# Optimization experiments

Hardware: AMD Instinct MI355X
Metric: run time of the kernel (lower is better)

## Reference

```python
import jax, jax.numpy as jnp
import numpy as np


def setup_inputs() -> dict:
    key = jax.random.key(0)
    ks = jax.random.split(key, 6)
    B, S, I, H = 64, 512, 1024, 1024
    sc = lambda *sh: 1.0 / np.sqrt(sh[0])
    return {
        "x": jax.random.normal(ks[0], (B, S, I), dtype=jnp.float32),
        "Wih": jax.random.normal(ks[1], (I, 4 * H), dtype=jnp.float32) * sc(I),
        "Whh": jax.random.normal(ks[2], (H, 4 * H), dtype=jnp.float32) * sc(H),
        "bih": jnp.zeros((4 * H,), dtype=jnp.float32),
        "bhh": jnp.zeros((4 * H,), dtype=jnp.float32),
        "Q": jax.random.normal(ks[3], (H, I), dtype=jnp.float32) * sc(H),
        "R": jax.random.normal(ks[4], (I, H), dtype=jnp.float32) * sc(I),
        "h0": jnp.zeros((B, H), dtype=jnp.float32),
        "c0": jnp.zeros((B, H), dtype=jnp.float32),
        "mog_iterations": 5,
    }


def reference(x, Wih, Whh, bih, bhh, Q, R, h0, c0, mog_iterations):
    # x: [B, S, I]; recurrence over S via lax.scan
    def step(carry, xt):
        ht, Ct = carry
        # mogrify: alternate rescaling of xt (odd i) and ht (even i)
        for i in range(1, mog_iterations + 1):
            if i % 2 == 0:
                ht = 2.0 * jax.nn.sigmoid(xt @ R) * ht
            else:
                xt = 2.0 * jax.nn.sigmoid(ht @ Q) * xt
        gates = xt @ Wih + bih + ht @ Whh + bhh  # [B, 4H]
        ig, fg, cg, og = jnp.split(gates, 4, axis=1)
        Ct = jax.nn.sigmoid(fg) * Ct + jax.nn.sigmoid(ig) * jnp.tanh(cg)
        ht = jax.nn.sigmoid(og) * jnp.tanh(Ct)
        return (ht, Ct), None

    xs = jnp.swapaxes(x, 0, 1)  # [S, B, I]
    (ht, Ct), _ = jax.lax.scan(step, (h0, c0), xs)
    return ht
```

## Files before the change

kernel.cpp:

```cpp
#include <hip/hip_runtime.h>
#include <stdint.h>

#define NBLK 256
#define NTHR 512
#define BATCH 64
#define HD 1024
#define SEQ 512

#define FLAG_STRIDE 32

typedef unsigned short u16;
typedef uint32_t u32;
typedef __attribute__((ext_vector_type(8))) short v8s;
typedef __attribute__((ext_vector_type(4))) float v4f;
typedef __attribute__((ext_vector_type(4))) unsigned int v4u;

__device__ __forceinline__ float bf2f(u16 u){
  union { float f; u32 i; } c; c.i = ((u32)u) << 16; return c.f;
}
__device__ __forceinline__ u16 f2bf(float f){
  union { float f; u32 i; } c; c.f = f;
  u32 i = c.i;
  return (u16)((i + 0x7fffu + ((i >> 16) & 1u)) >> 16);
}
__device__ __forceinline__ float sigm(float v){ return 1.f / (1.f + __expf(-v)); }

__device__ __forceinline__ u32 packf(float v){
  const u16 hi = f2bf(v);
  const u16 lo = f2bf(v - bf2f(hi));
  return (u32)hi | ((u32)lo << 16);
}
__device__ __forceinline__ float unpackf(u32 w){
  return bf2f((u16)(w & 0xffffu)) + bf2f((u16)(w >> 16));
}

__device__ __forceinline__ u32 ald(const u32* p){
  return __hip_atomic_load(p, __ATOMIC_RELAXED, __HIP_MEMORY_SCOPE_AGENT);
}
__device__ __forceinline__ void ast(u32* p, u32 v){
  __hip_atomic_store(p, v, __ATOMIC_RELAXED, __HIP_MEMORY_SCOPE_AGENT);
}
__device__ __forceinline__ int aldi(const int* p){
  return __hip_atomic_load(p, __ATOMIC_RELAXED, __HIP_MEMORY_SCOPE_AGENT);
}

__device__ __forceinline__ void ald_batch8(const u32* p, v4u r[8]){
  asm volatile(
    "global_load_dwordx4 %0, %8, off sc0 sc1\n\t"
    "global_load_dwordx4 %1, %8, off offset:16 sc0 sc1\n\t"
    "global_load_dwordx4 %2, %8, off offset:128 sc0 sc1\n\t"
    "global_load_dwordx4 %3, %8, off offset:144 sc0 sc1\n\t"
    "global_load_dwordx4 %4, %8, off offset:256 sc0 sc1\n\t"
    "global_load_dwordx4 %5, %8, off offset:272 sc0 sc1\n\t"
    "global_load_dwordx4 %6, %8, off offset:384 sc0 sc1\n\t"
    "global_load_dwordx4 %7, %8, off offset:400 sc0 sc1\n\t"
    "s_waitcnt vmcnt(0)"
    : "=&v"(r[0]), "=&v"(r[1]), "=&v"(r[2]), "=&v"(r[3]),
      "=&v"(r[4]), "=&v"(r[5]), "=&v"(r[6]), "=&v"(r[7])
    : "v"(p) : "memory");
}
__device__ __forceinline__ void ald_batch16(const u32* p, v4u r[16]){
  asm volatile(
    "global_load_dwordx4 %0, %16, off sc0 sc1\n\t"
    "global_load_dwordx4 %1, %16, off offset:16 sc0 sc1\n\t"
    "global_load_dwordx4 %2, %16, off offset:128 sc0 sc1\n\t"
    "global_load_dwordx4 %3, %16, off offset:144 sc0 sc1\n\t"
    "global_load_dwordx4 %4, %16, off offset:256 sc0 sc1\n\t"
    "global_load_dwordx4 %5, %16, off offset:272 sc0 sc1\n\t"
    "global_load_dwordx4 %6, %16, off offset:384 sc0 sc1\n\t"
    "global_load_dwordx4 %7, %16, off offset:400 sc0 sc1\n\t"
    "global_load_dwordx4 %8, %16, off offset:512 sc0 sc1\n\t"
    "global_load_dwordx4 %9, %16, off offset:528 sc0 sc1\n\t"
    "global_load_dwordx4 %10, %16, off offset:640 sc0 sc1\n\t"
    "global_load_dwordx4 %11, %16, off offset:656 sc0 sc1\n\t"
    "global_load_dwordx4 %12, %16, off offset:768 sc0 sc1\n\t"
    "global_load_dwordx4 %13, %16, off offset:784 sc0 sc1\n\t"
    "global_load_dwordx4 %14, %16, off offset:896 sc0 sc1\n\t"
    "global_load_dwordx4 %15, %16, off offset:912 sc0 sc1\n\t"
    "s_waitcnt vmcnt(0)"
    : "=&v"(r[0]), "=&v"(r[1]), "=&v"(r[2]), "=&v"(r[3]),
      "=&v"(r[4]), "=&v"(r[5]), "=&v"(r[6]), "=&v"(r[7]),
      "=&v"(r[8]), "=&v"(r[9]), "=&v"(r[10]), "=&v"(r[11]),
      "=&v"(r[12]), "=&v"(r[13]), "=&v"(r[14]), "=&v"(r[15])
    : "v"(p) : "memory");
}

struct FragPair { v8s hi; v8s lo; };
__device__ __forceinline__ FragPair splitpair(v4u w0, v4u w1){
  union { v8s v; u32 u[4]; } H, L;
#pragma unroll
  for (int i = 0; i < 2; i++){
    H.u[i]     = (w0[2*i] & 0xffffu) | (w0[2*i+1] << 16);
    L.u[i]     = (w0[2*i] >> 16)     | (w0[2*i+1] & 0xffff0000u);
    H.u[2 + i] = (w1[2*i] & 0xffffu) | (w1[2*i+1] << 16);
    L.u[2 + i] = (w1[2*i] >> 16)     | (w1[2*i+1] & 0xffff0000u);
  }
  FragPair f; f.hi = H.v; f.lo = L.v; return f;
}

__device__ __forceinline__ void gbar_all(int* flags, int target, int bid, int tid){
  __syncthreads();
  if (tid == 0)
    __hip_atomic_store(&flags[bid * FLAG_STRIDE], target, __ATOMIC_RELAXED, __HIP_MEMORY_SCOPE_AGENT);
  if (tid < 64){
    const int* p = flags + (tid * 4) * FLAG_STRIDE;
    for (;;){
      int a = aldi(p + 0 * FLAG_STRIDE), b = aldi(p + 1 * FLAG_STRIDE);
      int c = aldi(p + 2 * FLAG_STRIDE), d = aldi(p + 3 * FLAG_STRIDE);
      if (a >= target && b >= target && c >= target && d >= target) break;
      __builtin_amdgcn_s_sleep(1);
    }
  }
  __syncthreads();
}

__device__ __forceinline__ void gbar64(int* gf, int target, int member, int tid){
  __syncthreads();
  if (tid == 0)
    __hip_atomic_store(&gf[member * FLAG_STRIDE], target, __ATOMIC_RELAXED, __HIP_MEMORY_SCOPE_AGENT);
  if (tid < 64){
    while (aldi(&gf[tid * FLAG_STRIDE]) < target) __builtin_amdgcn_s_sleep(1);
  }
  __syncthreads();
}

struct MogPre { v8s bh[4]; v8s bl[4]; };
__device__ __forceinline__ MogPre mog_pre(const u16* WThi, const u16* WTlo, int cn, int tid){
  const int w = tid >> 6, lane = tid & 63;
  const int mi = lane & 15, q = lane >> 4;
  const int kb = w * 128 + q * 8;
  const u16* bh_p = WThi + (size_t)(cn + mi) * HD + kb;
  const u16* bl_p = WTlo + (size_t)(cn + mi) * HD + kb;
  MogPre pre;
#pragma unroll
  for (int ks = 0; ks < 4; ks++){
    pre.bh[ks] = *(const v8s*)(bh_p + ks * 32);
    pre.bl[ks] = *(const v8s*)(bl_p + ks * 32);
  }
  return pre;
}
struct GatesPre { v8s bh[4][2]; v8s bl[4][2]; };
__device__ __forceinline__ GatesPre gates_pre(
    const u16* WihThi, const u16* WihTlo,
    const u16* WhhThi, const u16* WhhTlo, int cn, int tid){
  const int w = tid >> 6, lane = tid & 63;
  const int mi = lane & 15, q = lane >> 4;
  const int src = w >> 2;
  const u16* Bh = src ? WhhThi : WihThi;
  const u16* Bl = src ? WhhTlo : WihTlo;
  const int kb = (w & 3) * 256 + q * 8;
  GatesPre g;
#pragma unroll
  for (int nt = 0; nt < 4; nt++){
    const size_t brow = (size_t)(nt * HD + cn + mi) * HD + kb;
#pragma unroll
    for (int ks = 0; ks < 2; ks++){
      g.bh[nt][ks] = *(const v8s*)(Bh + brow + ks * 32);
      g.bl[nt][ks] = *(const v8s*)(Bl + brow + ks * 32);
    }
  }
  return g;
}

__device__ __forceinline__ void mog_phase(
    MogPre pre, const u32* A,
    const float* multx, const u32* M, u32* O,
    int rm, int cn, int tid, float* cb)
{
  const int w = tid >> 6, lane = tid & 63;
  const int mi = lane & 15, q = lane >> 4;
  const int kb = w * 128 + q * 8;
  const int er = tid >> 4, ec = tid & 15;
  const int gi = (rm + er) * HD + (cn + ec);
  const bool epi = (tid < 256);
  float multv = 0.f; u32 mpack = 0;
  if (epi){
    if (multx) multv = __builtin_nontemporal_load(multx + (size_t)(rm + er) * (SEQ * HD) + (cn + ec));
    else       mpack = ald(M + gi);
  }
  v4u ar[8];
  ald_batch8(A + (size_t)(rm + mi) * HD + kb, ar);

  v4f acc = {0.f, 0.f, 0.f, 0.f};
#pragma unroll
  for (int ks = 0; ks < 4; ks++){
    FragPair a = splitpair(ar[2 * ks], ar[2 * ks + 1]);
    acc = __builtin_amdgcn_mfma_f32_16x16x32_bf16(a.hi, pre.bh[ks], acc, 0, 0, 0);
    acc = __builtin_amdgcn_mfma_f32_16x16x32_bf16(a.hi, pre.bl[ks], acc, 0, 0, 0);
    acc = __builtin_amdgcn_mfma_f32_16x16x32_bf16(a.lo, pre.bh[ks], acc, 0, 0, 0);
  }

  float* dst = cb + w * 1088;
#pragma unroll
  for (int r = 0; r < 4; r++) dst[(q * 4 + r) * 17 + mi] = acc[r];
  __syncthreads();
  if (epi){
    float v = 0.f;
#pragma unroll
    for (int w2 = 0; w2 < 8; w2++) v += cb[w2 * 1088 + er * 17 + ec];
    const float mult = multx ? multv : unpackf(mpack);
    ast(O + gi, packf(2.f * sigm(v) * mult));
  }
}

__device__ __forceinline__ void gates_phase(
    GatesPre gp, const u32* X, const u32* H,
    const u16* WihThi, const u16* WihTlo,
    const u16* WhhThi, const u16* WhhTlo,
    const float* bsum, float& creg, u32* O,
    int rm, int cn, int tid, float* cb, float* red)
{
  const int w = tid >> 6, lane = tid & 63;
  const int mi = lane & 15, q = lane >> 4;
  const int src = w >> 2;
  const u32* Ap = src ? H : X;
  const u16* Bh = src ? WhhThi : WihThi;
  const u16* Bl = src ? WhhTlo : WihTlo;
  const int kb = (w & 3) * 256 + q * 8;

  const u16* bh_p[4]; const u16* bl_p[4];
#pragma unroll
  for (int nt = 0; nt < 4; nt++){
    const size_t brow = (size_t)(nt * HD + cn + mi) * HD + kb;
    bh_p[nt] = Bh + brow; bl_p[nt] = Bl + brow;
  }
  v8s b2h[4], b2l[4];
#pragma unroll
  for (int nt = 0; nt < 4; nt++){
    b2h[nt] = *(const v8s*)(bh_p[nt] + 64);
    b2l[nt] = *(const v8s*)(bl_p[nt] + 64);
  }
  v4u ar[16];
  ald_batch16(Ap + (size_t)(rm + mi) * HD + kb, ar);

  v4f acc[4];
#pragma unroll
  for (int nt = 0; nt < 4; nt++) acc[nt] = (v4f){0.f, 0.f, 0.f, 0.f};
#pragma unroll
  for (int ks = 0; ks < 2; ks++){
    FragPair a = splitpair(ar[2 * ks], ar[2 * ks + 1]);
#pragma unroll
    for (int nt = 0; nt < 4; nt++){
      acc[nt] = __builtin_amdgcn_mfma_f32_16x16x32_bf16(a.hi, gp.bh[nt][ks], acc[nt], 0, 0, 0);
      acc[nt] = __builtin_amdgcn_mfma_f32_16x16x32_bf16(a.hi, gp.bl[nt][ks], acc[nt], 0, 0, 0);
      acc[nt] = __builtin_amdgcn_mfma_f32_16x16x32_bf16(a.lo, gp.bh[nt][ks], acc[nt], 0, 0, 0);
    }
  }
  {
    FragPair a = splitpair(ar[4], ar[5]);
#pragma unroll
    for (int nt = 0; nt < 4; nt++){
      acc[nt] = __builtin_amdgcn_mfma_f32_16x16x32_bf16(a.hi, b2h[nt], acc[nt], 0, 0, 0);
      acc[nt] = __builtin_amdgcn_mfma_f32_16x16x32_bf16(a.hi, b2l[nt], acc[nt], 0, 0, 0);
      acc[nt] = __builtin_amdgcn_mfma_f32_16x16x32_bf16(a.lo, b2h[nt], acc[nt], 0, 0, 0);
    }
  }
#pragma unroll
  for (int ks = 3; ks < 8; ks++){
    const int k = ks * 32;
    FragPair a = splitpair(ar[2 * ks], ar[2 * ks + 1]);
#pragma unroll
    for (int nt = 0; nt < 4; nt++){
      v8s bh = *(const v8s*)(bh_p[nt] + k);
      v8s bl = *(const v8s*)(bl_p[nt] + k);
      acc[nt] = __builtin_amdgcn_mfma_f32_16x16x32_bf16(a.hi, bh, acc[nt], 0, 0, 0);
      acc[nt] = __builtin_amdgcn_mfma_f32_16x16x32_bf16(a.hi, bl, acc[nt], 0, 0, 0);
      acc[nt] = __builtin_amdgcn_mfma_f32_16x16x32_bf16(a.lo, bh, acc[nt], 0, 0, 0);
    }
  }
#pragma unroll
  for (int nt = 0; nt < 4; nt++)
#pragma unroll
    for (int r = 0; r < 4; r++)
      cb[(w * 4 + nt) * 272 + (q * 4 + r) * 17 + mi] = acc[nt][r];
  __syncthreads();
  for (int e = tid; e < 1024; e += NTHR){
    const int qq = e >> 8, rc = e & 255, r = rc >> 4, c = rc & 15;
    float v = 0.f;
#pragma unroll
    for (int w2 = 0; w2 < 8; w2++) v += cb[(w2 * 4 + qq) * 272 + r * 17 + c];
    red[qq * 272 + r * 17 + c] = v;
  }
  __syncthreads();
  if (tid < 256){
    const int r = tid >> 4, c = tid & 15;
    const float g0 = red[0 * 272 + r * 17 + c] + bsum[0];
    const float g1 = red[1 * 272 + r * 17 + c] + bsum[1];
    const float g2 = red[2 * 272 + r * 17 + c] + bsum[2];
    const float g3 = red[3 * 272 + r * 17 + c] + bsum[3];
    const float ig = sigm(g0), fg = sigm(g1), cg = tanhf(g2), og = sigm(g3);
    const float cnew = fg * creg + ig * cg;
    creg = cnew;
    const float h = og * tanhf(cnew);
    ast(O + (rm + r) * HD + (cn + c), packf(h));
  }
}

extern "C" __global__ void __launch_bounds__(NTHR, 2)
moglstm_kernel(const float* __restrict__ x, const float* __restrict__ Wih,
               const float* __restrict__ Whh, const float* __restrict__ bih,
               const float* __restrict__ bhh, const float* __restrict__ Q,
               const float* __restrict__ Rw, const float* __restrict__ h0,
               const float* __restrict__ c0, float* __restrict__ out,
               uint8_t* __restrict__ ws)
{
  __shared__ float cb[32 * 272];
  __shared__ float red[4 * 272];
  __shared__ u16 shh[32 * 33], shl[32 * 33];

  uint8_t* p = ws;
  u32* xA   = (u32*)p;     p += (size_t)BATCH * HD * 4;
  u32* xB   = (u32*)p;     p += (size_t)BATCH * HD * 4;
  u32* hA   = (u32*)p;     p += (size_t)BATCH * HD * 4;
  u32* hB   = (u32*)p;     p += (size_t)BATCH * HD * 4;
  u16* QThi  = (u16*)p;    p += (size_t)HD * HD * 2;
  u16* QTlo  = (u16*)p;    p += (size_t)HD * HD * 2;
  u16* RThi  = (u16*)p;    p += (size_t)HD * HD * 2;
  u16* RTlo  = (u16*)p;    p += (size_t)HD * HD * 2;
  u16* WihThi = (u16*)p;   p += (size_t)4 * HD * HD * 2;
  u16* WihTlo = (u16*)p;   p += (size_t)4 * HD * HD * 2;
  u16* WhhThi = (u16*)p;   p += (size_t)4 * HD * HD * 2;
  u16* WhhTlo = (u16*)p;   p += (size_t)4 * HD * HD * 2;
  int* flagsP = (int*)p;
  int* gfbase = flagsP + 256 * FLAG_STRIDE;

  const int bid = blockIdx.x, tid = threadIdx.x;
  const int group = bid >> 6, member = bid & 63;
  const int rm = group * 16, cn = member * 16;
  int* gf = gfbase + group * (64 * FLAG_STRIDE);

  for (int tile = bid; tile < 10240; tile += NBLK){
    const float* W; u16 *Th, *Tl; int N, kt, nt;
    if (tile < 1024)      { W = Q;   Th = QThi;   Tl = QTlo;   N = HD;     int tl = tile;        kt = tl >> 5; nt = tl & 31; }
    else if (tile < 2048) { W = Rw;  Th = RThi;   Tl = RTlo;   N = HD;     int tl = tile - 1024; kt = tl >> 5; nt = tl & 31; }
    else if (tile < 6144) { W = Wih; Th = WihThi; Tl = WihTlo; N = 4 * HD; int tl = tile - 2048; kt = tl >> 7; nt = tl & 127; }
    else                  { W = Whh; Th = WhhThi; Tl = WhhTlo; N = 4 * HD; int tl = tile - 6144; kt = tl >> 7; nt = tl & 127; }
    for (int e = tid; e < 1024; e += NTHR){
      const int ki = e >> 5, nj = e & 31;
      const float v = W[(size_t)(kt * 32 + ki) * N + nt * 32 + nj];
      const u16 hi = f2bf(v);
      shh[ki * 33 + nj] = hi;
      shl[ki * 33 + nj] = f2bf(v - bf2f(hi));
    }
    __syncthreads();
    for (int e = tid; e < 1024; e += NTHR){
      const int ni = e >> 5, kj = e & 31;
      Th[(size_t)(nt * 32 + ni) * HD + kt * 32 + kj] = shh[kj * 33 + ni];
      Tl[(size_t)(nt * 32 + ni) * HD + kt * 32 + kj] = shl[kj * 33 + ni];
    }
    __syncthreads();
  }
  for (int i = bid * NTHR + tid; i < BATCH * HD; i += NBLK * NTHR)
    hA[i] = packf(h0[i]);

  float creg = 0.f;
  float bsum[4] = {0.f, 0.f, 0.f, 0.f};
  if (tid < 256){
    const int r = tid >> 4, c = tid & 15, col = cn + c;
    creg = c0[(rm + r) * HD + col];
#pragma unroll
    for (int qq = 0; qq < 4; qq++) bsum[qq] = bih[qq * HD + col] + bhh[qq * HD + col];
  }

  __threadfence();
  gbar_all(flagsP, 1, bid, tid);

  u32 *hc = hA, *ho = hB;
  int bar = 0;
  MogPre pre = mog_pre(QThi, QTlo, cn, tid);
  for (int t = 0; t < SEQ; t++){
    mog_phase(pre, hc, x + (size_t)t * HD, nullptr, xA, rm, cn, tid, cb);
    pre = mog_pre(RThi, RTlo, cn, tid);
    bar++; gbar64(gf, bar, member, tid);
    mog_phase(pre, xA, nullptr, hc, ho, rm, cn, tid, cb);
    pre = mog_pre(QThi, QTlo, cn, tid);
    bar++; gbar64(gf, bar, member, tid);
    mog_phase(pre, ho, nullptr, xA, xB, rm, cn, tid, cb);
    pre = mog_pre(RThi, RTlo, cn, tid);
    bar++; gbar64(gf, bar, member, tid);
    mog_phase(pre, xB, nullptr, ho, hc, rm, cn, tid, cb);
    pre = mog_pre(QThi, QTlo, cn, tid);
    bar++; gbar64(gf, bar, member, tid);
    mog_phase(pre, hc, nullptr, xB, xA, rm, cn, tid, cb);
    GatesPre gp = gates_pre(WihThi, WihTlo, WhhThi, WhhTlo, cn, tid);
    bar++; gbar64(gf, bar, member, tid);
    gates_phase(gp, xA, hc, WihThi, WihTlo, WhhThi, WhhTlo, bsum, creg, ho,
                rm, cn, tid, cb, red);
    pre = mog_pre(QThi, QTlo, cn, tid);
    bar++; gbar64(gf, bar, member, tid);
    u32* tswp = hc; hc = ho; ho = tswp;
  }

  if (tid < 256){
    const int er = tid >> 4, ec = tid & 15;
    const int gi = (rm + er) * HD + (cn + ec);
    out[gi] = unpackf(ald(hc + gi));
  }
}

extern "C" void kernel_launch(void* const* d_in, const int* in_sizes, int n_in,
                              void* d_out, int out_size, void* d_ws, size_t ws_size,
                              hipStream_t stream)
{
  const float* x   = (const float*)d_in[0];
  const float* Wih = (const float*)d_in[1];
  const float* Whh = (const float*)d_in[2];
  const float* bih = (const float*)d_in[3];
  const float* bhh = (const float*)d_in[4];
  const float* Q   = (const float*)d_in[5];
  const float* Rw  = (const float*)d_in[6];
  const float* h0  = (const float*)d_in[7];
  const float* c0  = (const float*)d_in[8];
  float* out = (float*)d_out;
  uint8_t* ws = (uint8_t*)d_ws;
  void* args[] = { &x, &Wih, &Whh, &bih, &bhh, &Q, &Rw, &h0, &c0, &out, &ws };
  hipLaunchCooperativeKernel((void*)moglstm_kernel, dim3(NBLK), dim3(NTHR),
                             args, 0, stream);
}
```

Measured before the change: 21.50 ms.

## Replace group barriers with fine-grained per-producer flag waits inside phases

Removes the 64-block group barrier between mogrifier and gate phases. Each wave now spins only on the flags of the blocks that produced the K-slice of the activation it is about to load, and each phase publishes its completion flag at the end. This is meant to let blocks start a phase as soon as their specific inputs are ready instead of waiting for the whole group, and it overlaps epilogue multiplier loads with the wait. The risk is correctness around WAR hazards on reused buffers (xA/xB/hc/ho), since producers no longer wait for all consumers before overwriting. It also adds flag zeroing whose ordering relative to the initial barrier matters.

```diff
diff --git a/kernel.cpp b/kernel.cpp
--- a/kernel.cpp
+++ b/kernel.cpp
@@ -114,16 +114,6 @@
   __syncthreads();
 }
 
-__device__ __forceinline__ void gbar64(int* gf, int target, int member, int tid){
-  __syncthreads();
-  if (tid == 0)
-    __hip_atomic_store(&gf[member * FLAG_STRIDE], target, __ATOMIC_RELAXED, __HIP_MEMORY_SCOPE_AGENT);
-  if (tid < 64){
-    while (aldi(&gf[tid * FLAG_STRIDE]) < target) __builtin_amdgcn_s_sleep(1);
-  }
-  __syncthreads();
-}
-
 struct MogPre { v8s bh[4]; v8s bl[4]; };
 __device__ __forceinline__ MogPre mog_pre(const u16* WThi, const u16* WTlo, int cn, int tid){
   const int w = tid >> 6, lane = tid & 63;
@@ -163,9 +153,9 @@
 }
 
 __device__ __forceinline__ void mog_phase(
-    MogPre pre, const u32* A,
+    MogPre pre, const u32* A, int donebar,
     const float* multx, const u32* M, u32* O,
-    int rm, int cn, int tid, float* cb)
+    int rm, int cn, int tid, float* cb, int* gf, int member)
 {
   const int w = tid >> 6, lane = tid & 63;
   const int mi = lane & 15, q = lane >> 4;
@@ -178,6 +168,11 @@
     if (multx) multv = __builtin_nontemporal_load(multx + (size_t)(rm + er) * (SEQ * HD) + (cn + ec));
     else       mpack = ald(M + gi);
   }
+  {
+    const int abar = donebar - 1;
+    const int* fp = gf + (8 * w + (lane & 7)) * FLAG_STRIDE;
+    while (aldi(fp) < abar) __builtin_amdgcn_s_sleep(1);
+  }
   v4u ar[8];
   ald_batch8(A + (size_t)(rm + mi) * HD + kb, ar);
 
@@ -201,14 +196,17 @@
     const float mult = multx ? multv : unpackf(mpack);
     ast(O + gi, packf(2.f * sigm(v) * mult));
   }
+  __syncthreads();
+  if (tid == 0)
+    __hip_atomic_store(&gf[member * FLAG_STRIDE], donebar, __ATOMIC_RELAXED, __HIP_MEMORY_SCOPE_AGENT);
 }
 
 __device__ __forceinline__ void gates_phase(
-    GatesPre gp, const u32* X, const u32* H,
+    GatesPre gp, const u32* X, const u32* H, int donebar,
     const u16* WihThi, const u16* WihTlo,
     const u16* WhhThi, const u16* WhhTlo,
     const float* bsum, float& creg, u32* O,
-    int rm, int cn, int tid, float* cb, float* red)
+    int rm, int cn, int tid, float* cb, float* red, int* gf, int member)
 {
   const int w = tid >> 6, lane = tid & 63;
   const int mi = lane & 15, q = lane >> 4;
@@ -229,6 +227,11 @@
   for (int nt = 0; nt < 4; nt++){
     b2h[nt] = *(const v8s*)(bh_p[nt] + 64);
     b2l[nt] = *(const v8s*)(bl_p[nt] + 64);
+  }
+  if (!src){
+    const int abar = donebar - 1;
+    const int* fp = gf + ((w & 3) * 16 + (lane & 15)) * FLAG_STRIDE;
+    while (aldi(fp) < abar) __builtin_amdgcn_s_sleep(1);
   }
   v4u ar[16];
   ald_batch16(Ap + (size_t)(rm + mi) * HD + kb, ar);
@@ -294,6 +297,9 @@
     const float h = og * tanhf(cnew);
     ast(O + (rm + r) * HD + (cn + c), packf(h));
   }
+  __syncthreads();
+  if (tid == 0)
+    __hip_atomic_store(&gf[member * FLAG_STRIDE], donebar, __ATOMIC_RELAXED, __HIP_MEMORY_SCOPE_AGENT);
 }
 
 extern "C" __global__ void __launch_bounds__(NTHR, 2)
@@ -352,6 +358,8 @@
   }
   for (int i = bid * NTHR + tid; i < BATCH * HD; i += NBLK * NTHR)
     hA[i] = packf(h0[i]);
+  for (int i = bid * NTHR + tid; i < 4 * 64 * FLAG_STRIDE; i += NBLK * NTHR)
+    gfbase[i] = 0;
 
   float creg = 0.f;
   float bsum[4] = {0.f, 0.f, 0.f, 0.f};
@@ -369,25 +377,25 @@
   int bar = 0;
   MogPre pre = mog_pre(QThi, QTlo, cn, tid);
   for (int t = 0; t < SEQ; t++){
-    mog_phase(pre, hc, x + (size_t)t * HD, nullptr, xA, rm, cn, tid, cb);
+    bar++;
+    mog_phase(pre, hc, bar, x + (size_t)t * HD, nullptr, xA, rm, cn, tid, cb, gf, member);
     pre = mog_pre(RThi, RTlo, cn, tid);
-    bar++; gbar64(gf, bar, member, tid);
-    mog_phase(pre, xA, nullptr, hc, ho, rm, cn, tid, cb);
+    bar++;
+    mog_phase(pre, xA, bar, nullptr, hc, ho, rm, cn, tid, cb, gf, member);
     pre = mog_pre(QThi, QTlo, cn, tid);
-    bar++; gbar64(gf, bar, member, tid);
-    mog_phase(pre, ho, nullptr, xA, xB, rm, cn, tid, cb);
+    bar++;
+    mog_phase(pre, ho, bar, nullptr, xA, xB, rm, cn, tid, cb, gf, member);
     pre = mog_pre(RThi, RTlo, cn, tid);
-    bar++; gbar64(gf, bar, member, tid);
-    mog_phase(pre, xB, nullptr, ho, hc, rm, cn, tid, cb);
+    bar++;
+    mog_phase(pre, xB, bar, nullptr, ho, hc, rm, cn, tid, cb, gf, member);
     pre = mog_pre(QThi, QTlo, cn, tid);
-    bar++; gbar64(gf, bar, member, tid);
-    mog_phase(pre, hc, nullptr, xB, xA, rm, cn, tid, cb);
+    bar++;
+    mog_phase(pre, hc, bar, nullptr, xB, xA, rm, cn, tid, cb, gf, member);
     GatesPre gp = gates_pre(WihThi, WihTlo, WhhThi, WhhTlo, cn, tid);
-    bar++; gbar64(gf, bar, member, tid);
-    gates_phase(gp, xA, hc, WihThi, WihTlo, WhhThi, WhhTlo, bsum, creg, ho,
-                rm, cn, tid, cb, red);
+    bar++;
+    gates_phase(gp, xA, hc, bar, WihThi, WihTlo, WhhThi, WhhTlo, bsum, creg, ho,
+                rm, cn, tid, cb, red, gf, member);
     pre = mog_pre(QThi, QTlo, cn, tid);
-    bar++; gbar64(gf, bar, member, tid);
     u32* tswp = hc; hc = ho; ho = tswp;
   }
 
```

Measured after the change: 21.34 ms. Within noise of the previous version (-0.7%).

## Replace group flag barriers with per-element tagged data polling

Applied to the files above, without the earlier changes.

Removes the per-phase 64-block flag barriers and instead stores each activation value together with a timestep tag, so consumers spin directly on the data they need until tags match. Intermediate buffers are double-buffered by timestep parity so that no barrier is needed between steps. The initial barrier becomes a cooperative grid sync, and the final output is written directly in the last step. This doubles the bytes moved per activation and relies on the 8-byte store landing atomically so value and tag are seen together, in exchange for finer-grained dataflow synchronization.

```diff
diff --git a/kernel.cpp b/kernel.cpp
--- a/kernel.cpp
+++ b/kernel.cpp
@@ -1,4 +1,5 @@
 #include <hip/hip_runtime.h>
+#include <hip/hip_cooperative_groups.h>
 #include <stdint.h>
 
 #define NBLK 256
@@ -7,13 +8,12 @@
 #define HD 1024
 #define SEQ 512
 
-#define FLAG_STRIDE 32
-
 typedef unsigned short u16;
 typedef uint32_t u32;
 typedef __attribute__((ext_vector_type(8))) short v8s;
 typedef __attribute__((ext_vector_type(4))) float v4f;
 typedef __attribute__((ext_vector_type(4))) unsigned int v4u;
+typedef __attribute__((ext_vector_type(2))) unsigned int v2u;
 
 __device__ __forceinline__ float bf2f(u16 u){
   union { float f; u32 i; } c; c.i = ((u32)u) << 16; return c.f;
@@ -37,46 +37,31 @@
 __device__ __forceinline__ u32 ald(const u32* p){
   return __hip_atomic_load(p, __ATOMIC_RELAXED, __HIP_MEMORY_SCOPE_AGENT);
 }
-__device__ __forceinline__ void ast(u32* p, u32 v){
-  __hip_atomic_store(p, v, __ATOMIC_RELAXED, __HIP_MEMORY_SCOPE_AGENT);
-}
-__device__ __forceinline__ int aldi(const int* p){
-  return __hip_atomic_load(p, __ATOMIC_RELAXED, __HIP_MEMORY_SCOPE_AGENT);
-}
-
-__device__ __forceinline__ void ald_batch8(const u32* p, v4u r[8]){
-  asm volatile(
-    "global_load_dwordx4 %0, %8, off sc0 sc1\n\t"
-    "global_load_dwordx4 %1, %8, off offset:16 sc0 sc1\n\t"
-    "global_load_dwordx4 %2, %8, off offset:128 sc0 sc1\n\t"
-    "global_load_dwordx4 %3, %8, off offset:144 sc0 sc1\n\t"
-    "global_load_dwordx4 %4, %8, off offset:256 sc0 sc1\n\t"
-    "global_load_dwordx4 %5, %8, off offset:272 sc0 sc1\n\t"
-    "global_load_dwordx4 %6, %8, off offset:384 sc0 sc1\n\t"
-    "global_load_dwordx4 %7, %8, off offset:400 sc0 sc1\n\t"
-    "s_waitcnt vmcnt(0)"
-    : "=&v"(r[0]), "=&v"(r[1]), "=&v"(r[2]), "=&v"(r[3]),
-      "=&v"(r[4]), "=&v"(r[5]), "=&v"(r[6]), "=&v"(r[7])
-    : "v"(p) : "memory");
-}
-__device__ __forceinline__ void ald_batch16(const u32* p, v4u r[16]){
+
+__device__ __forceinline__ void past(u32* pb, int gi, u32 val, int tag){
+  v2u d; d[0] = val; d[1] = (u32)tag;
+  asm volatile("global_store_dwordx2 %0, %1, off sc0 sc1"
+               :: "v"(pb + 2 * (size_t)gi), "v"(d) : "memory");
+}
+
+__device__ __forceinline__ void pald16(const u32* p, v4u r[16]){
   asm volatile(
     "global_load_dwordx4 %0, %16, off sc0 sc1\n\t"
     "global_load_dwordx4 %1, %16, off offset:16 sc0 sc1\n\t"
-    "global_load_dwordx4 %2, %16, off offset:128 sc0 sc1\n\t"
-    "global_load_dwordx4 %3, %16, off offset:144 sc0 sc1\n\t"
+    "global_load_dwordx4 %2, %16, off offset:32 sc0 sc1\n\t"
+    "global_load_dwordx4 %3, %16, off offset:48 sc0 sc1\n\t"
     "global_load_dwordx4 %4, %16, off offset:256 sc0 sc1\n\t"
     "global_load_dwordx4 %5, %16, off offset:272 sc0 sc1\n\t"
-    "global_load_dwordx4 %6, %16, off offset:384 sc0 sc1\n\t"
-    "global_load_dwordx4 %7, %16, off offset:400 sc0 sc1\n\t"
+    "global_load_dwordx4 %6, %16, off offset:288 sc0 sc1\n\t"
+    "global_load_dwordx4 %7, %16, off offset:304 sc0 sc1\n\t"
     "global_load_dwordx4 %8, %16, off offset:512 sc0 sc1\n\t"
     "global_load_dwordx4 %9, %16, off offset:528 sc0 sc1\n\t"
-    "global_load_dwordx4 %10, %16, off offset:640 sc0 sc1\n\t"
-    "global_load_dwordx4 %11, %16, off offset:656 sc0 sc1\n\t"
+    "global_load_dwordx4 %10, %16, off offset:544 sc0 sc1\n\t"
+    "global_load_dwordx4 %11, %16, off offset:560 sc0 sc1\n\t"
     "global_load_dwordx4 %12, %16, off offset:768 sc0 sc1\n\t"
     "global_load_dwordx4 %13, %16, off offset:784 sc0 sc1\n\t"
-    "global_load_dwordx4 %14, %16, off offset:896 sc0 sc1\n\t"
-    "global_load_dwordx4 %15, %16, off offset:912 sc0 sc1\n\t"
+    "global_load_dwordx4 %14, %16, off offset:800 sc0 sc1\n\t"
+    "global_load_dwordx4 %15, %16, off offset:816 sc0 sc1\n\t"
     "s_waitcnt vmcnt(0)"
     : "=&v"(r[0]), "=&v"(r[1]), "=&v"(r[2]), "=&v"(r[3]),
       "=&v"(r[4]), "=&v"(r[5]), "=&v"(r[6]), "=&v"(r[7]),
@@ -85,6 +70,25 @@
     : "v"(p) : "memory");
 }
 
+__device__ __forceinline__ void poll16(const u32* p, int utag, v4u ar[8]){
+  const u32 ut = (u32)utag;
+  v4u r[16];
+  int tries = 0;
+  for (;;){
+    pald16(p, r);
+    bool ok = true;
+#pragma unroll
+    for (int i = 0; i < 16; i++) ok &= (r[i][1] == ut) & (r[i][3] == ut);
+    if (__all(ok)) break;
+    if (++tries > 1) __builtin_amdgcn_s_sleep(2);
+  }
+#pragma unroll
+  for (int ks = 0; ks < 4; ks++){
+    ar[2*ks]   = (v4u){ r[4*ks][0],   r[4*ks][2],   r[4*ks+1][0], r[4*ks+1][2] };
+    ar[2*ks+1] = (v4u){ r[4*ks+2][0], r[4*ks+2][2], r[4*ks+3][0], r[4*ks+3][2] };
+  }
+}
+
 struct FragPair { v8s hi; v8s lo; };
 __device__ __forceinline__ FragPair splitpair(v4u w0, v4u w1){
   union { v8s v; u32 u[4]; } H, L;
@@ -96,32 +100,6 @@
     L.u[2 + i] = (w1[2*i] >> 16)     | (w1[2*i+1] & 0xffff0000u);
   }
   FragPair f; f.hi = H.v; f.lo = L.v; return f;
-}
-
-__device__ __forceinline__ void gbar_all(int* flags, int target, int bid, int tid){
-  __syncthreads();
-  if (tid == 0)
-    __hip_atomic_store(&flags[bid * FLAG_STRIDE], target, __ATOMIC_RELAXED, __HIP_MEMORY_SCOPE_AGENT);
-  if (tid < 64){
-    const int* p = flags + (tid * 4) * FLAG_STRIDE;
-    for (;;){
-      int a = aldi(p + 0 * FLAG_STRIDE), b = aldi(p + 1 * FLAG_STRIDE);
-      int c = aldi(p + 2 * FLAG_STRIDE), d = aldi(p + 3 * FLAG_STRIDE);
-      if (a >= target && b >= target && c >= target && d >= target) break;
-      __builtin_amdgcn_s_sleep(1);
-    }
-  }
-  __syncthreads();
-}
-
-__device__ __forceinline__ void gbar64(int* gf, int target, int member, int tid){
-  __syncthreads();
-  if (tid == 0)
-    __hip_atomic_store(&gf[member * FLAG_STRIDE], target, __ATOMIC_RELAXED, __HIP_MEMORY_SCOPE_AGENT);
-  if (tid < 64){
-    while (aldi(&gf[tid * FLAG_STRIDE]) < target) __builtin_amdgcn_s_sleep(1);
-  }
-  __syncthreads();
 }
 
 struct MogPre { v8s bh[4]; v8s bl[4]; };
@@ -163,8 +141,8 @@
 }
 
 __device__ __forceinline__ void mog_phase(
-    MogPre pre, const u32* A,
-    const float* multx, const u32* M, u32* O,
+    MogPre pre, const u32* Ap, int utag,
+    const float* multx, const u32* Mp, u32* Op, int otag,
     int rm, int cn, int tid, float* cb)
 {
   const int w = tid >> 6, lane = tid & 63;
@@ -176,10 +154,10 @@
   float multv = 0.f; u32 mpack = 0;
   if (epi){
     if (multx) multv = __builtin_nontemporal_load(multx + (size_t)(rm + er) * (SEQ * HD) + (cn + ec));
-    else       mpack = ald(M + gi);
+    else       mpack = ald(Mp + 2 * (size_t)gi);
   }
   v4u ar[8];
-  ald_batch8(A + (size_t)(rm + mi) * HD + kb, ar);
+  poll16(Ap + 2 * ((size_t)(rm + mi) * HD + kb), utag, ar);
 
   v4f acc = {0.f, 0.f, 0.f, 0.f};
 #pragma unroll
@@ -199,73 +177,70 @@
 #pragma unroll
     for (int w2 = 0; w2 < 8; w2++) v += cb[w2 * 1088 + er * 17 + ec];
     const float mult = multx ? multv : unpackf(mpack);
-    ast(O + gi, packf(2.f * sigm(v) * mult));
-  }
+    past(Op, gi, packf(2.f * sigm(v) * mult), otag);
+  }
+  __syncthreads();
 }
 
 __device__ __forceinline__ void gates_phase(
-    GatesPre gp, const u32* X, const u32* H,
+    GatesPre gp, const u32* Xp, const u32* Hp, int utag,
     const u16* WihThi, const u16* WihTlo,
     const u16* WhhThi, const u16* WhhTlo,
-    const float* bsum, float& creg, u32* O,
+    const float* bsum, float& creg, u32* Ohp, int otag,
+    float* out, bool last,
     int rm, int cn, int tid, float* cb, float* red)
 {
   const int w = tid >> 6, lane = tid & 63;
   const int mi = lane & 15, q = lane >> 4;
   const int src = w >> 2;
-  const u32* Ap = src ? H : X;
+  const u32* Ap = src ? Hp : Xp;
   const u16* Bh = src ? WhhThi : WihThi;
   const u16* Bl = src ? WhhTlo : WihTlo;
   const int kb = (w & 3) * 256 + q * 8;
-
   const u16* bh_p[4]; const u16* bl_p[4];
 #pragma unroll
   for (int nt = 0; nt < 4; nt++){
     const size_t brow = (size_t)(nt * HD + cn + mi) * HD + kb;
     bh_p[nt] = Bh + brow; bl_p[nt] = Bl + brow;
   }
-  v8s b2h[4], b2l[4];
-#pragma unroll
-  for (int nt = 0; nt < 4; nt++){
-    b2h[nt] = *(const v8s*)(bh_p[nt] + 64);
-    b2l[nt] = *(const v8s*)(bl_p[nt] + 64);
-  }
-  v4u ar[16];
-  ald_batch16(Ap + (size_t)(rm + mi) * HD + kb, ar);
+  const u32* abase = Ap + 2 * ((size_t)(rm + mi) * HD + kb);
 
   v4f acc[4];
 #pragma unroll
   for (int nt = 0; nt < 4; nt++) acc[nt] = (v4f){0.f, 0.f, 0.f, 0.f};
-#pragma unroll
-  for (int ks = 0; ks < 2; ks++){
-    FragPair a = splitpair(ar[2 * ks], ar[2 * ks + 1]);
-#pragma unroll
-    for (int nt = 0; nt < 4; nt++){
-      acc[nt] = __builtin_amdgcn_mfma_f32_16x16x32_bf16(a.hi, gp.bh[nt][ks], acc[nt], 0, 0, 0);
-      acc[nt] = __builtin_amdgcn_mfma_f32_16x16x32_bf16(a.hi, gp.bl[nt][ks], acc[nt], 0, 0, 0);
-      acc[nt] = __builtin_amdgcn_mfma_f32_16x16x32_bf16(a.lo, gp.bh[nt][ks], acc[nt], 0, 0, 0);
-    }
-  }
+
   {
-    FragPair a = splitpair(ar[4], ar[5]);
-#pragma unroll
-    for (int nt = 0; nt < 4; nt++){
-      acc[nt] = __builtin_amdgcn_mfma_f32_16x16x32_bf16(a.hi, b2h[nt], acc[nt], 0, 0, 0);
-      acc[nt] = __builtin_amdgcn_mfma_f32_16x16x32_bf16(a.hi, b2l[nt], acc[nt], 0, 0, 0);
-      acc[nt] = __builtin_amdgcn_mfma_f32_16x16x32_bf16(a.lo, b2h[nt], acc[nt], 0, 0, 0);
-    }
-  }
-#pragma unroll
-  for (int ks = 3; ks < 8; ks++){
-    const int k = ks * 32;
-    FragPair a = splitpair(ar[2 * ks], ar[2 * ks + 1]);
-#pragma unroll
-    for (int nt = 0; nt < 4; nt++){
-      v8s bh = *(const v8s*)(bh_p[nt] + k);
-      v8s bl = *(const v8s*)(bl_p[nt] + k);
-      acc[nt] = __builtin_amdgcn_mfma_f32_16x16x32_bf16(a.hi, bh, acc[nt], 0, 0, 0);
-      acc[nt] = __builtin_amdgcn_mfma_f32_16x16x32_bf16(a.hi, bl, acc[nt], 0, 0, 0);
-      acc[nt] = __builtin_amdgcn_mfma_f32_16x16x32_bf16(a.lo, bh, acc[nt], 0, 0, 0);
+    v4u ar[8];
+    poll16(abase, utag, ar);
+#pragma unroll
+    for (int ks = 0; ks < 4; ks++){
+      FragPair a = splitpair(ar[2 * ks], ar[2 * ks + 1]);
+#pragma unroll
+      for (int nt = 0; nt < 4; nt++){
+        v8s bh, bl;
+        if (ks < 2){ bh = gp.bh[nt][ks]; bl = gp.bl[nt][ks]; }
+        else       { bh = *(const v8s*)(bh_p[nt] + ks * 32);
+                     bl = *(const v8s*)(bl_p[nt] + ks * 32); }
+        acc[nt] = __builtin_amdgcn_mfma_f32_16x16x32_bf16(a.hi, bh, acc[nt], 0, 0, 0);
+        acc[nt] = __builtin_amdgcn_mfma_f32_16x16x32_bf16(a.hi, bl, acc[nt], 0, 0, 0);
+        acc[nt] = __builtin_amdgcn_mfma_f32_16x16x32_bf16(a.lo, bh, acc[nt], 0, 0, 0);
+      }
+    }
+  }
+  {
+    v4u ar[8];
+    poll16(abase + 256, utag, ar);
+#pragma unroll
+    for (int ks = 4; ks < 8; ks++){
+      FragPair a = splitpair(ar[2 * (ks - 4)], ar[2 * (ks - 4) + 1]);
+#pragma unroll
+      for (int nt = 0; nt < 4; nt++){
+        v8s bh = *(const v8s*)(bh_p[nt] + ks * 32);
+        v8s bl = *(const v8s*)(bl_p[nt] + ks * 32);
+        acc[nt] = __builtin_amdgcn_mfma_f32_16x16x32_bf16(a.hi, bh, acc[nt], 0, 0, 0);
+        acc[nt] = __builtin_amdgcn_mfma_f32_16x16x32_bf16(a.hi, bl, acc[nt], 0, 0, 0);
+        acc[nt] = __builtin_amdgcn_mfma_f32_16x16x32_bf16(a.lo, bh, acc[nt], 0, 0, 0);
+      }
     }
   }
 #pragma unroll
@@ -292,8 +267,11 @@
     const float cnew = fg * creg + ig * cg;
     creg = cnew;
     const float h = og * tanhf(cnew);
-    ast(O + (rm + r) * HD + (cn + c), packf(h));
-  }
+    const int gi = (rm + r) * HD + (cn + c);
+    past(Ohp, gi, packf(h), otag);
+    if (last) out[gi] = h;
+  }
+  __syncthreads();
 }
 
 extern "C" __global__ void __launch_bounds__(NTHR, 2)
@@ -308,26 +286,28 @@
   __shared__ float red[4 * 272];
   __shared__ u16 shh[32 * 33], shl[32 * 33];
 
-  uint8_t* p = ws;
-  u32* xA   = (u32*)p;     p += (size_t)BATCH * HD * 4;
-  u32* xB   = (u32*)p;     p += (size_t)BATCH * HD * 4;
-  u32* hA   = (u32*)p;     p += (size_t)BATCH * HD * 4;
-  u32* hB   = (u32*)p;     p += (size_t)BATCH * HD * 4;
-  u16* QThi  = (u16*)p;    p += (size_t)HD * HD * 2;
-  u16* QTlo  = (u16*)p;    p += (size_t)HD * HD * 2;
-  u16* RThi  = (u16*)p;    p += (size_t)HD * HD * 2;
-  u16* RTlo  = (u16*)p;    p += (size_t)HD * HD * 2;
-  u16* WihThi = (u16*)p;   p += (size_t)4 * HD * HD * 2;
-  u16* WihTlo = (u16*)p;   p += (size_t)4 * HD * HD * 2;
-  u16* WhhThi = (u16*)p;   p += (size_t)4 * HD * HD * 2;
-  u16* WhhTlo = (u16*)p;   p += (size_t)4 * HD * HD * 2;
-  int* flagsP = (int*)p;
-  int* gfbase = flagsP + 256 * FLAG_STRIDE;
+  const size_t SB = (size_t)BATCH * HD * 2;
+  u32* P = (u32*)ws;
+  u32* x1[2] = { P + 0 * SB, P + 1 * SB };
+  u32* h1[2] = { P + 2 * SB, P + 3 * SB };
+  u32* x2[2] = { P + 4 * SB, P + 5 * SB };
+  u32* h2[2] = { P + 6 * SB, P + 7 * SB };
+  u32* x3[2] = { P + 8 * SB, P + 9 * SB };
+  u32* hst0  = P + 10 * SB;
+  u32* hst1  = P + 11 * SB;
+  uint8_t* p = (uint8_t*)(P + 12 * SB);
+  u16* QThi  = (u16*)p;  p += (size_t)HD * HD * 2;
+  u16* QTlo  = (u16*)p;  p += (size_t)HD * HD * 2;
+  u16* RThi  = (u16*)p;  p += (size_t)HD * HD * 2;
+  u16* RTlo  = (u16*)p;  p += (size_t)HD * HD * 2;
+  u16* WihThi = (u16*)p; p += (size_t)4 * HD * HD * 2;
+  u16* WihTlo = (u16*)p; p += (size_t)4 * HD * HD * 2;
+  u16* WhhThi = (u16*)p; p += (size_t)4 * HD * HD * 2;
+  u16* WhhTlo = (u16*)p; p += (size_t)4 * HD * HD * 2;
 
   const int bid = blockIdx.x, tid = threadIdx.x;
   const int group = bid >> 6, member = bid & 63;
   const int rm = group * 16, cn = member * 16;
-  int* gf = gfbase + group * (64 * FLAG_STRIDE);
 
   for (int tile = bid; tile < 10240; tile += NBLK){
     const float* W; u16 *Th, *Tl; int N, kt, nt;
@@ -350,8 +330,14 @@
     }
     __syncthreads();
   }
-  for (int i = bid * NTHR + tid; i < BATCH * HD; i += NBLK * NTHR)
-    hA[i] = packf(h0[i]);
+  for (size_t i = (size_t)bid * NTHR + tid; i < 11 * SB; i += (size_t)NBLK * NTHR)
+    P[i] = 0xFFFFFFFFu;
+  for (int e = bid * NTHR + tid; e < BATCH * HD; e += NBLK * NTHR){
+    hst1[2 * e]     = packf(h0[e]);
+    hst1[2 * e + 1] = 0u;
+  }
+  __threadfence();
+  cooperative_groups::this_grid().sync();
 
   float creg = 0.f;
   float bsum[4] = {0.f, 0.f, 0.f, 0.f};
@@ -362,39 +348,28 @@
     for (int qq = 0; qq < 4; qq++) bsum[qq] = bih[qq * HD + col] + bhh[qq * HD + col];
   }
 
-  __threadfence();
-  gbar_all(flagsP, 1, bid, tid);
-
-  u32 *hc = hA, *ho = hB;
-  int bar = 0;
   MogPre pre = mog_pre(QThi, QTlo, cn, tid);
   for (int t = 0; t < SEQ; t++){
-    mog_phase(pre, hc, x + (size_t)t * HD, nullptr, xA, rm, cn, tid, cb);
+    const int pbit = t & 1;
+    const u32* hrd = pbit ? hst0 : hst1;
+    u32*       hwr = pbit ? hst1 : hst0;
+    u32 *x1p = x1[pbit], *h1p = h1[pbit], *x2p = x2[pbit], *h2p = h2[pbit], *x3p = x3[pbit];
+    const int tg = t + 1;
+
+    mog_phase(pre, hrd, t, x + (size_t)t * HD, nullptr, x1p, tg, rm, cn, tid, cb);
     pre = mog_pre(RThi, RTlo, cn, tid);
-    bar++; gbar64(gf, bar, member, tid);
-    mog_phase(pre, xA, nullptr, hc, ho, rm, cn, tid, cb);
+    mog_phase(pre, x1p, tg, nullptr, hrd, h1p, tg, rm, cn, tid, cb);
     pre = mog_pre(QThi, QTlo, cn, tid);
-    bar++; gbar64(gf, bar, member, tid);
-    mog_phase(pre, ho, nullptr, xA, xB, rm, cn, tid, cb);
+    mog_phase(pre, h1p, tg, nullptr, x1p, x2p, tg, rm, cn, tid, cb);
     pre = mog_pre(RThi, RTlo, cn, tid);
-    bar++; gbar64(gf, bar, member, tid);
-    mog_phase(pre, xB, nullptr, ho, hc, rm, cn, tid, cb);
+    mog_phase(pre, x2p, tg, nullptr, h1p, h2p, tg, rm, cn, tid, cb);
     pre = mog_pre(QThi, QTlo, cn, tid);
-    bar++; gbar64(gf, bar, member, tid);
-    mog_phase(pre, hc, nullptr, xB, xA, rm, cn, tid, cb);
+    mog_phase(pre, h2p, tg, nullptr, x2p, x3p, tg, rm, cn, tid, cb);
     GatesPre gp = gates_pre(WihThi, WihTlo, WhhThi, WhhTlo, cn, tid);
-    bar++; gbar64(gf, bar, member, tid);
-    gates_phase(gp, xA, hc, WihThi, WihTlo, WhhThi, WhhTlo, bsum, creg, ho,
+    gates_phase(gp, x3p, h2p, tg, WihThi, WihTlo, WhhThi, WhhTlo,
+                bsum, creg, hwr, tg, out, (t == SEQ - 1),
                 rm, cn, tid, cb, red);
     pre = mog_pre(QThi, QTlo, cn, tid);
-    bar++; gbar64(gf, bar, member, tid);
-    u32* tswp = hc; hc = ho; ho = tswp;
-  }
-
-  if (tid < 256){
-    const int er = tid >> 4, ec = tid & 15;
-    const int gi = (rm + er) * HD + (cn + ec);
-    out[gi] = unpackf(ald(hc + gi));
   }
 }
 
```

After: 29.78 ms. 1.39x slower.
